# Kernel optimization log

Hardware: AMD Instinct MI355X
Metric: run time of the kernel (lower is better)

The kernel has to match this reference:

```python
import math
import jax, jax.numpy as jnp
import numpy as np

SCALES = (128.0, 256.0, 512.0)
ASPECT_RATIOS = (0.5, 1.0, 2.0)
NMS_THR = 0.7
PRENMS_K = 6000   # rpn_test_prenms_topk (module built with training=False)
POST_K = 300      # rpn_test_topk
MIN_SIZE = 16.0
DW_CLIP = math.log(1000.0 / 16.0)


def conv2d(x, w, b, pad):
    y = jax.lax.conv_general_dilated(
        x, w, window_strides=(1, 1), padding=[(pad, pad), (pad, pad)],
        dimension_numbers=("NCHW", "OIHW", "NCHW"))
    return y + b[None, :, None, None]


def generate_anchors(im_h, im_w, grid_h, grid_w, dtype):
    stride_h = float(im_h // grid_h)
    stride_w = float(im_w // grid_w)
    ar = jnp.asarray(ASPECT_RATIOS, dtype)
    sc = jnp.asarray(SCALES, dtype)
    h_ratios = jnp.sqrt(ar)
    w_ratios = 1.0 / h_ratios
    hs = (h_ratios[:, None] * sc[None, :]).reshape(-1)   # [A]
    ws = (w_ratios[:, None] * sc[None, :]).reshape(-1)
    base = jnp.round(jnp.stack([-ws, -hs, ws, hs], axis=1) / 2.0)  # [A,4]
    xs = jnp.arange(grid_w, dtype=dtype) * stride_w
    ys = jnp.arange(grid_h, dtype=dtype) * stride_h
    sy, sx = jnp.meshgrid(ys, xs, indexing="ij")
    sx = sx.reshape(-1); sy = sy.reshape(-1)
    shift = jnp.stack([sx, sy, sx, sy], axis=1)           # [HW,4]
    return (shift[:, None, :] + base[None, :, :]).reshape(-1, 4)  # [HW*A,4]


def decode_boxes(pred, anchors):
    # pred, anchors: [N,4] -> decoded [N,4]
    w = anchors[:, 2] - anchors[:, 0]
    h = anchors[:, 3] - anchors[:, 1]
    cx = anchors[:, 0] + 0.5 * w
    cy = anchors[:, 1] + 0.5 * h
    dx, dy = pred[:, 0], pred[:, 1]
    dw = jnp.minimum(pred[:, 2], DW_CLIP)
    dh = jnp.minimum(pred[:, 3], DW_CLIP)
    px = dx * w + cx
    py = dy * h + cy
    pw = jnp.exp(dw) * w
    ph = jnp.exp(dh) * h
    return jnp.stack([px - 0.5 * pw, py - 0.5 * ph, px + 0.5 * pw, py + 0.5 * ph], axis=1)


def nms_keep(boxes, valid, thr):
    # boxes assumed sorted by descending score; sequential greedy NMS.
    N = boxes.shape[0]
    area = (boxes[:, 2] - boxes[:, 0]) * (boxes[:, 3] - boxes[:, 1])
    idx = jnp.arange(N)

    def body(i, keep):
        b = jax.lax.dynamic_slice(boxes, (i, 0), (1, 4))[0]
        x1 = jnp.maximum(b[0], boxes[:, 0])
        y1 = jnp.maximum(b[1], boxes[:, 1])
        x2 = jnp.minimum(b[2], boxes[:, 2])
        y2 = jnp.minimum(b[3], boxes[:, 3])
        inter = jnp.clip(x2 - x1, 0.0) * jnp.clip(y2 - y1, 0.0)
        iou = inter / (area[i] + area - inter)
        suppress = (iou > thr) & (idx > i) & keep[i]
        return keep & ~suppress

    return jax.lax.fori_loop(0, N, body, valid)


def rpn_forward(image, feat, rpn_conv_w, rpn_conv_b, cls_w, cls_b, bbox_w, bbox_b):
    rpn_feat = jax.nn.relu(conv2d(feat, rpn_conv_w, rpn_conv_b, pad=1))
    cls_scores = conv2d(rpn_feat, cls_w, cls_b, pad=0)       # [B,A,H,W]
    box_pred = conv2d(rpn_feat, bbox_w, bbox_b, pad=0)       # [B,4A,H,W]
    B, A, H, W = cls_scores.shape
    im_h, im_w = image.shape[-2], image.shape[-1]
    anchors = generate_anchors(im_h, im_w, H, W, feat.dtype)  # [HWA,4]

    cls_flat = jnp.transpose(cls_scores, (0, 2, 3, 1)).reshape(-1)              # [B*H*W*A]
    pred = jnp.transpose(box_pred.reshape(B, A, 4, H, W), (0, 3, 4, 1, 2)).reshape(-1, 4)
    proposals = decode_boxes(pred, anchors)                   # [N,4]

    scores = jax.nn.sigmoid(cls_flat)
    top_scores, top_idx = jax.lax.top_k(scores, PRENMS_K)
    props = proposals[top_idx]                                # [K,4]
    # clamp to image boundary
    props = jnp.stack([
        jnp.clip(props[:, 0], 0.0, float(im_w)),
        jnp.clip(props[:, 1], 0.0, float(im_h)),
        jnp.clip(props[:, 2], 0.0, float(im_w)),
        jnp.clip(props[:, 3], 0.0, float(im_h))], axis=1)
    w = props[:, 2] - props[:, 0]
    h = props[:, 3] - props[:, 1]
    valid = (w >= MIN_SIZE) & (h >= MIN_SIZE)
    keep = nms_keep(props, valid, NMS_THR)                    # already score-sorted
    masked = jnp.where(keep, top_scores, -jnp.inf)
    final_scores, sel = jax.lax.top_k(masked, POST_K)
    final_boxes = props[sel]
    ok = jnp.isfinite(final_scores)
    final_boxes = jnp.where(ok[:, None], final_boxes, 0.0)
    final_scores = jnp.where(ok, final_scores, 0.0)
    return jnp.concatenate([final_boxes, final_scores[:, None]], axis=1)  # [POST_K,5]


def setup_inputs() -> dict:
    key = jax.random.key(0)
    ks = jax.random.split(key, 6)
    C, H, W, A = 256, 128, 128, 9
    IMH = IMW = 1024
    std = 0.01
    return {
        "image": jax.random.normal(ks[0], (1, 3, IMH, IMW), jnp.float32),
        "feat": jax.random.normal(ks[1], (1, C, H, W), jnp.float32),
        "rpn_conv_w": jax.random.normal(ks[2], (C, C, 3, 3), jnp.float32) * std,
        "rpn_conv_b": jnp.zeros((C,), jnp.float32),
        "cls_w": jax.random.normal(ks[3], (A, C, 1, 1), jnp.float32) * std,
        "cls_b": jnp.zeros((A,), jnp.float32),
        "bbox_w": jax.random.normal(ks[4], (4 * A, C, 1, 1), jnp.float32) * std,
        "bbox_b": jnp.zeros((4 * A,), jnp.float32),
    }


def reference(image, feat, rpn_conv_w, rpn_conv_b, cls_w, cls_b, bbox_w, bbox_b):
    return rpn_forward(image, feat, rpn_conv_w, rpn_conv_b, cls_w, cls_b, bbox_w, bbox_b)
```

## Files before the change

### kernel.cpp

```cpp
#include <hip/hip_runtime.h>

#define HW 128
#define NPIX 16384
#define CIN 256
#define NSC 147456
#define PRENMS 6000
#define POSTK 300
#define DW_CLIP_F 4.135166556742356f
#define MW 96
typedef unsigned long long ull;

__global__ void prep_kernel(const float* __restrict__ w, float* __restrict__ wt,
                            const float* __restrict__ cls_w, const float* __restrict__ bbox_w,
                            float* __restrict__ wh45,
                            unsigned* __restrict__ zp, int nz) {
    int i = blockIdx.x * 256 + threadIdx.x;
    if (i < nz) zp[i] = 0u;
    if (i < 11520) {
        int ci = i / 45, s = i - ci * 45;
        wh45[i] = (s < 9) ? cls_w[s * CIN + ci] : bbox_w[(s - 9) * CIN + ci];
    }
    if (i < 2304 * 256) {
        int k = i >> 8, co = i & 255;
        wt[i] = w[co * 2304 + k];
    }
}

__global__ __launch_bounds__(256) void conv3x3_kernel(
    const float* __restrict__ feat, const float* __restrict__ wt,
    float* __restrict__ part)
{
    const int tx = threadIdx.x, ty = threadIdx.y;
    const int x0 = blockIdx.x * 16, y0 = blockIdx.y * 16;
    const int h = blockIdx.z >> 4;
    const int co0 = (blockIdx.z & 15) << 4;
    const int px = x0 + tx, py = y0 + ty;

    float acc[16];
#pragma unroll
    for (int i = 0; i < 16; ++i) acc[i] = 0.f;

    const float* fh = feat + h * 128 * NPIX;
    const float* wh = wt + h * 128 * 9 * 256 + co0;

    const bool interior = (x0 > 0) && (y0 > 0) && (x0 < 112) && (y0 < 112);

    if (interior) {
        const float* fb = fh + (py - 1) * 128 + (px - 1);
#pragma unroll 2
        for (int ci = 0; ci < 128; ++ci) {
            const float* f = fb + ci * NPIX;
            float v[9];
#pragma unroll
            for (int t = 0; t < 9; ++t) {
                const int ky = t / 3, kx = t - ky * 3;
                v[t] = f[ky * 128 + kx];
            }
            const float* wp = wh + ci * 9 * 256;
#pragma unroll
            for (int t = 0; t < 9; ++t) {
#pragma unroll
                for (int co = 0; co < 16; ++co)
                    acc[co] = fmaf(v[t], wp[t * 256 + co], acc[co]);
            }
        }
    } else {
        int off[9];
        float okf[9];
#pragma unroll
        for (int t = 0; t < 9; ++t) {
            const int ky = t / 3 - 1, kx = t - (t / 3) * 3 - 1;
            const int gy = py + ky, gx = px + kx;
            const bool ok = ((unsigned)gy < 128u) && ((unsigned)gx < 128u);
            off[t] = ok ? (gy * 128 + gx) : 0;
            okf[t] = ok ? 1.f : 0.f;
        }
#pragma unroll 2
        for (int ci = 0; ci < 128; ++ci) {
            const float* f = fh + ci * NPIX;
            float v[9];
#pragma unroll
            for (int t = 0; t < 9; ++t) v[t] = f[off[t]] * okf[t];
            const float* wp = wh + ci * 9 * 256;
#pragma unroll
            for (int t = 0; t < 9; ++t) {
#pragma unroll
                for (int co = 0; co < 16; ++co)
                    acc[co] = fmaf(v[t], wp[t * 256 + co], acc[co]);
            }
        }
    }
    float* po = part + h * (CIN * NPIX) + co0 * NPIX + py * 128 + px;
#pragma unroll
    for (int co = 0; co < 16; ++co)
        po[co * NPIX] = acc[co];
}

__global__ __launch_bounds__(256) void heads_kernel(
    const float* __restrict__ part, const float* __restrict__ conv_b,
    const float* __restrict__ wh45,
    const float* __restrict__ cls_b, const float* __restrict__ bbox_b,
    float* __restrict__ scores, float* __restrict__ bb)
{
    __shared__ float partial[3][64][46];
    const int t = threadIdx.x;
    const int lane = t & 63, q = t >> 6;
    const int p = blockIdx.x * 64 + lane;
    const float* p0 = part + p;
    const float* p1 = part + CIN * NPIX + p;
    const int cb = q * 64;

    float acc[45];
#pragma unroll
    for (int i = 0; i < 45; ++i) acc[i] = 0.f;

    float va[4], vb[4];
#pragma unroll
    for (int k = 0; k < 4; ++k) {
        va[k] = p0[(cb + k) * NPIX];
        vb[k] = p1[(cb + k) * NPIX];
    }
#pragma unroll 4
    for (int i = 0; i < 64; ++i) {
        const int ci = cb + i;
        float v = fmaxf(va[i & 3] + vb[i & 3] + conv_b[ci], 0.f);
        if (i + 4 < 64) {
            va[i & 3] = p0[(ci + 4) * NPIX];
            vb[i & 3] = p1[(ci + 4) * NPIX];
        }
        const float* wr = wh45 + ci * 45;
#pragma unroll
        for (int s = 0; s < 45; ++s)
            acc[s] = fmaf(v, wr[s], acc[s]);
    }
    if (q) {
#pragma unroll
        for (int s = 0; s < 45; ++s) partial[q - 1][lane][s] = acc[s];
    }
    __syncthreads();
    if (q == 0) {
#pragma unroll
        for (int s = 0; s < 45; ++s) {
            float r = acc[s] + partial[0][lane][s];
            r += partial[1][lane][s];
            r += partial[2][lane][s];
            acc[s] = r;
        }
#pragma unroll
        for (int a = 0; a < 9; ++a) {
            float s = acc[a] + cls_b[a];
            scores[p * 9 + a] = 1.0f / (1.0f + expf(-s));
        }
#pragma unroll
        for (int c = 0; c < 36; ++c) {
            bb[c * NPIX + p] = acc[9 + c] + bbox_b[c];
        }
    }
}

__global__ __launch_bounds__(1024) void hist1_kernel(const float* __restrict__ scores,
                                                     unsigned* __restrict__ hist1,
                                                     unsigned* __restrict__ meta) {
    __shared__ unsigned h[16384];
    __shared__ unsigned lastflag;
    const int tid = threadIdx.x;
    for (int i = tid; i < 16384; i += 1024) h[i] = 0u;
    __syncthreads();
    for (int i = blockIdx.x * 1024 + tid; i < NSC; i += 64 * 1024) {
        atomicAdd(&h[__float_as_uint(scores[i]) >> 16], 1u);
    }
    __syncthreads();
    for (int i = tid; i < 16384; i += 1024) {
        unsigned c = h[i];
        if (c) atomicAdd(&hist1[i], c);
    }
    __threadfence();
    if (tid == 0) lastflag = (atomicAdd(&meta[4], 1u) == 63u) ? 1u : 0u;
    __syncthreads();
    if (!lastflag) return;
    const volatile unsigned* vh = (const volatile unsigned*)hist1;
    unsigned local[16];
    unsigned s = 0;
#pragma unroll
    for (int i = 0; i < 16; ++i) { local[i] = vh[tid * 16 + i]; s += local[i]; }
    __syncthreads();
    h[tid] = s;
    __syncthreads();
    for (int off = 1; off < 1024; off <<= 1) {
        unsigned v = h[tid] + ((tid + off < 1024) ? h[tid + off] : 0u);
        __syncthreads();
        h[tid] = v;
        __syncthreads();
    }
    unsigned run = h[tid] - s;
#pragma unroll
    for (int i = 15; i >= 0; --i) {
        unsigned nb = run + local[i];
        if (nb >= (unsigned)PRENMS && run < (unsigned)PRENMS) {
            meta[1] = (unsigned)(tid * 16 + i);
            meta[2] = run;
        }
        run = nb;
    }
}

__global__ __launch_bounds__(1024) void hist2_kernel(const float* __restrict__ scores,
                                                     unsigned* __restrict__ meta,
                                                     unsigned* __restrict__ hist2) {
    __shared__ unsigned ss[1024];
    __shared__ unsigned lastflag;
    const int tid = threadIdx.x;
    const unsigned b1 = meta[1];
    for (int i = blockIdx.x * 1024 + tid; i < NSC; i += 64 * 1024) {
        unsigned bits = __float_as_uint(scores[i]);
        if ((bits >> 16) == b1) atomicAdd(&hist2[bits & 0xFFFFu], 1u);
    }
    __threadfence();
    if (tid == 0) lastflag = (atomicAdd(&meta[5], 1u) == 63u) ? 1u : 0u;
    __syncthreads();
    if (!lastflag) return;
    const volatile unsigned* vh = (const volatile unsigned*)hist2;
    const unsigned need = (unsigned)PRENMS - meta[2];
    unsigned local[64];
    unsigned s = 0;
    for (int i = 0; i < 64; ++i) { local[i] = vh[tid * 64 + i]; s += local[i]; }
    ss[tid] = s;
    __syncthreads();
    for (int off = 1; off < 1024; off <<= 1) {
        unsigned v = ss[tid] + ((tid + off < 1024) ? ss[tid + off] : 0u);
        __syncthreads();
        ss[tid] = v;
        __syncthreads();
    }
    unsigned run = ss[tid] - s;
    for (int i = 63; i >= 0; --i) {
        unsigned nb = run + local[i];
        if (nb >= need && run < need) {
            meta[3] = (b1 << 16) | (unsigned)(tid * 64 + i);
        }
        run = nb;
    }
}

__global__ void compact_kernel(const float* __restrict__ scores, unsigned* __restrict__ meta,
                               ull* __restrict__ cand) {
    int i = blockIdx.x * 256 + threadIdx.x;
    unsigned bits = (i < NSC) ? __float_as_uint(scores[i]) : 0u;
    bool pred = (i < NSC) && (bits >= meta[3]);
    ull bal = __ballot(pred);
    int lane = threadIdx.x & 63;
    unsigned cnt = (unsigned)__popcll(bal);
    unsigned base = 0;
    if (lane == 0 && cnt) base = atomicAdd(&meta[0], cnt);
    base = __shfl(base, 0);
    if (pred) {
        unsigned off = (unsigned)__popcll(bal & ((1ull << lane) - 1ull));
        unsigned pos = base + off;
        if (pos < 8192u)
            cand[pos] = ((ull)bits << 32) | (unsigned)(~i);
    }
}

__global__ __launch_bounds__(1024) void sortA_kernel(const ull* __restrict__ cand,
                                                     const unsigned* __restrict__ meta,
                                                     ull* __restrict__ sorted) {
    __shared__ ull keys[2048];
    const int tid = threadIdx.x;
    const int base = blockIdx.x * 2048;
    const int n = min((int)meta[0], 8192);
    for (int i = tid; i < 2048; i += 1024) {
        int g = base + i;
        keys[i] = (g < n) ? cand[g] : (ull)(8191 - g);
    }
    __syncthreads();
    for (int k = 2; k <= 2048; k <<= 1) {
        for (int j = k >> 1; j >= 1; j >>= 1) {
            int s = tid;
            int i = ((s & ~(j - 1)) << 1) | (s & (j - 1));
            int p = i | j;
            ull a = keys[i], c = keys[p];
            bool desc = ((i & k) == 0);
            bool sw = desc ? (a < c) : (a > c);
            if (sw) { keys[i] = c; keys[p] = a; }
            __syncthreads();
        }
    }
    for (int i = tid; i < 2048; i += 1024) sorted[base + i] = keys[i];
}

__global__ __launch_bounds__(256) void merge_decode_kernel(
    const ull* __restrict__ sorted, const float* __restrict__ bb,
    float* __restrict__ selbox, float* __restrict__ selsc,
    ull* __restrict__ validbits)
{
    const int g = blockIdx.x * 256 + threadIdx.x;
    ull key = sorted[g];
    const int c = g >> 11;
    int rank = g & 2047;
#pragma unroll
    for (int cc = 0; cc < 4; ++cc) {
        if (cc == c) continue;
        const ull* arr = sorted + cc * 2048;
        int lo = 0, hi = 2048;
        while (lo < hi) { int mid = (lo + hi) >> 1; if (arr[mid] > key) lo = mid + 1; else hi = mid; }
        rank += lo;
    }
    if (rank >= PRENMS) return;
    unsigned sbits = (unsigned)(key >> 32);
    unsigned idx = ~(unsigned)(key & 0xFFFFFFFFull);
    float score = __uint_as_float(sbits);
    int p = (int)(idx / 9u);
    int a = (int)(idx - (unsigned)p * 9u);
    int y = p >> 7, x = p & 127;
    float d0 = bb[(a * 4 + 0) * NPIX + p];
    float d1 = bb[(a * 4 + 1) * NPIX + p];
    float d2 = bb[(a * 4 + 2) * NPIX + p];
    float d3 = bb[(a * 4 + 3) * NPIX + p];
    int ar_i = a / 3, sc_i = a - ar_i * 3;
    float arv = (ar_i == 0) ? 0.5f : ((ar_i == 1) ? 1.0f : 2.0f);
    float scv = (sc_i == 0) ? 128.f : ((sc_i == 1) ? 256.f : 512.f);
    float hr = sqrtf(arv);
    float wr = 1.0f / hr;
    float hs = hr * scv;
    float wsv = wr * scv;
    float bx1 = rintf(-wsv * 0.5f), by1 = rintf(-hs * 0.5f);
    float bx2 = rintf(wsv * 0.5f),  by2 = rintf(hs * 0.5f);
    float ax1 = x * 8.f + bx1, ay1 = y * 8.f + by1;
    float ax2 = x * 8.f + bx2, ay2 = y * 8.f + by2;
    float wa = ax2 - ax1, ha = ay2 - ay1;
    float cx = ax1 + 0.5f * wa, cy = ay1 + 0.5f * ha;
    float dw = fminf(d2, DW_CLIP_F), dh = fminf(d3, DW_CLIP_F);
    float px = d0 * wa + cx, py = d1 * ha + cy;
    float pw = expf(dw) * wa, ph = expf(dh) * ha;
    float x1 = px - 0.5f * pw, y1 = py - 0.5f * ph;
    float x2 = px + 0.5f * pw, y2 = py + 0.5f * ph;
    x1 = fminf(fmaxf(x1, 0.f), 1024.f);
    y1 = fminf(fmaxf(y1, 0.f), 1024.f);
    x2 = fminf(fmaxf(x2, 0.f), 1024.f);
    y2 = fminf(fmaxf(y2, 0.f), 1024.f);
    float bw = x2 - x1, bh = y2 - y1;
    selbox[rank * 4 + 0] = x1; selbox[rank * 4 + 1] = y1;
    selbox[rank * 4 + 2] = x2; selbox[rank * 4 + 3] = y2;
    selsc[rank] = score;
    if ((bw >= 16.f) && (bh >= 16.f))
        atomicOr(&validbits[rank >> 6], 1ull << (rank & 63));
}

__global__ __launch_bounds__(256) void maskbuild_kernel(
    const float* __restrict__ selbox, ull* __restrict__ mask)
{
    __shared__ float jb0[64], jb1[64], jb2[64], jb3[64];
    const int jw = blockIdx.y;
    const int tid = threadIdx.x;
    const int i = blockIdx.x * 256 + tid;
    if (jw * 64 + 63 < blockIdx.x * 256) {
        if (i < PRENMS) mask[(size_t)i * MW + jw] = 0ull;
        return;
    }
    if (tid < 64) {
        int j = jw * 64 + tid;
        float x1 = 0.f, y1 = 0.f, x2 = 0.f, y2 = 0.f;
        if (j < PRENMS) {
            x1 = selbox[j * 4 + 0]; y1 = selbox[j * 4 + 1];
            x2 = selbox[j * 4 + 2]; y2 = selbox[j * 4 + 3];
        }
        jb0[tid] = x1; jb1[tid] = y1; jb2[tid] = x2; jb3[tid] = y2;
    }
    __syncthreads();
    if (i >= PRENMS) return;
    const float ix1 = selbox[i * 4 + 0], iy1 = selbox[i * 4 + 1];
    const float ix2 = selbox[i * 4 + 2], iy2 = selbox[i * 4 + 3];
    const float iarea = (ix2 - ix1) * (iy2 - iy1);
    ull word = 0ull;
    for (int b = 0; b < 64; ++b) {
        int j = jw * 64 + b;
        float xx1 = fmaxf(ix1, jb0[b]);
        float yy1 = fmaxf(iy1, jb1[b]);
        float xx2 = fminf(ix2, jb2[b]);
        float yy2 = fminf(iy2, jb3[b]);
        float iw = fmaxf(xx2 - xx1, 0.f);
        float ih = fmaxf(yy2 - yy1, 0.f);
        float inter = iw * ih;
        float jarea = (jb2[b] - jb0[b]) * (jb3[b] - jb1[b]);
        float iou = inter / (iarea + jarea - inter);
        if (j > i && iou > 0.7f) word |= (1ull << b);
    }
    mask[(size_t)i * MW + jw] = word;
}

__global__ __launch_bounds__(64) void nms_scan_kernel(
    const ull* __restrict__ validbits,
    const ull* __restrict__ mask,
    const float* __restrict__ selbox, const float* __restrict__ selsc,
    float* __restrict__ out)
{
    __shared__ int kept[POSTK];
    const int l = threadIdx.x;
    ull supp0 = ~validbits[l];
    ull supp1 = (l < 30) ? ~validbits[64 + l] : ~0ull;
    int nk = 0;
    ull ownrow_next = mask[(size_t)l * MW + 0];
    for (int wi = 0; wi < 94 && nk < POSTK; ++wi) {
        ull ownrow = ownrow_next;
        if (wi < 93) ownrow_next = mask[(size_t)((wi + 1) * 64 + l) * MW + (wi + 1)];
        ull wsup = (wi < 64) ? __shfl(supp0, wi) : __shfl(supp1, wi - 64);
        ull active = ~wsup;
        if (!active) continue;
        ull keptbits = 0ull;
        while (active && nk < POSTK) {
            int b = __builtin_ctzll(active);
            keptbits |= (1ull << b);
            if (l == 0) kept[nk] = wi * 64 + b;
            nk++;
            ull rowb = __shfl(ownrow, b);
            ull gt = (b == 63) ? 0ull : (~0ull << (b + 1));
            active &= gt & ~rowb;
        }
        while (keptbits) {
            int b0 = __builtin_ctzll(keptbits); keptbits &= keptbits - 1;
            int b1 = -1, b2 = -1, b3 = -1;
            if (keptbits) { b1 = __builtin_ctzll(keptbits); keptbits &= keptbits - 1; }
            if (keptbits) { b2 = __builtin_ctzll(keptbits); keptbits &= keptbits - 1; }
            if (keptbits) { b3 = __builtin_ctzll(keptbits); keptbits &= keptbits - 1; }
            const ull* r0 = mask + (size_t)(wi * 64 + b0) * MW;
            ull t0a = r0[l], t0b = (l < 30) ? r0[64 + l] : 0ull;
            ull t1a = 0, t1b = 0, t2a = 0, t2b = 0, t3a = 0, t3b = 0;
            if (b1 >= 0) { const ull* r1 = mask + (size_t)(wi * 64 + b1) * MW; t1a = r1[l]; t1b = (l < 30) ? r1[64 + l] : 0ull; }
            if (b2 >= 0) { const ull* r2 = mask + (size_t)(wi * 64 + b2) * MW; t2a = r2[l]; t2b = (l < 30) ? r2[64 + l] : 0ull; }
            if (b3 >= 0) { const ull* r3 = mask + (size_t)(wi * 64 + b3) * MW; t3a = r3[l]; t3b = (l < 30) ? r3[64 + l] : 0ull; }
            supp0 |= t0a | t1a | t2a | t3a;
            supp1 |= t0b | t1b | t2b | t3b;
        }
    }
    __syncthreads();
    for (int r = l; r < POSTK; r += 64) {
        if (r < nk) {
            int i = kept[r];
            out[r * 5 + 0] = selbox[i * 4 + 0];
            out[r * 5 + 1] = selbox[i * 4 + 1];
            out[r * 5 + 2] = selbox[i * 4 + 2];
            out[r * 5 + 3] = selbox[i * 4 + 3];
            out[r * 5 + 4] = selsc[i];
        } else {
            out[r * 5 + 0] = 0.f; out[r * 5 + 1] = 0.f;
            out[r * 5 + 2] = 0.f; out[r * 5 + 3] = 0.f;
            out[r * 5 + 4] = 0.f;
        }
    }
}

extern "C" void kernel_launch(void* const* d_in, const int* in_sizes, int n_in,
                              void* d_out, int out_size, void* d_ws, size_t ws_size,
                              hipStream_t stream) {
    const float* feat    = (const float*)d_in[1];
    const float* conv_w  = (const float*)d_in[2];
    const float* conv_b  = (const float*)d_in[3];
    const float* cls_w   = (const float*)d_in[4];
    const float* cls_b   = (const float*)d_in[5];
    const float* bbox_w  = (const float*)d_in[6];
    const float* bbox_b  = (const float*)d_in[7];
    float* out = (float*)d_out;

    char* ws = (char*)d_ws;
    float*    part      = (float*)(ws + 0);
    float*    wt        = (float*)(ws + 33554432);
    float*    wh45      = (float*)(ws + 35913728);
    float*    bb        = (float*)(ws + 35959808);
    float*    scores    = (float*)(ws + 38319104);
    unsigned* hist1     = (unsigned*)(ws + 38908928);
    unsigned* hist2     = (unsigned*)(ws + 38974464);
    unsigned* meta      = (unsigned*)(ws + 39236608);
    ull*      validbits = (ull*)(ws + 39236864);
    ull*      cand      = (ull*)(ws + 39237632);
    ull*      sorted    = (ull*)(ws + 39303168);
    float*    selbox    = (float*)(ws + 39368704);
    float*    selsc     = (float*)(ws + 39464960);
    ull*      mask      = (ull*)(ws + 39489024);

    const int nz = 16384 + 65536 + 64 + 192;
    prep_kernel<<<2304, 256, 0, stream>>>(conv_w, wt, cls_w, bbox_w, wh45, hist1, nz);
    conv3x3_kernel<<<dim3(8, 8, 32), dim3(16, 16), 0, stream>>>(feat, wt, part);
    heads_kernel<<<256, 256, 0, stream>>>(part, conv_b, wh45, cls_b, bbox_b, scores, bb);
    hist1_kernel<<<64, 1024, 0, stream>>>(scores, hist1, meta);
    hist2_kernel<<<64, 1024, 0, stream>>>(scores, meta, hist2);
    compact_kernel<<<(NSC + 255) / 256, 256, 0, stream>>>(scores, meta, cand);
    sortA_kernel<<<4, 1024, 0, stream>>>(cand, meta, sorted);
    merge_decode_kernel<<<32, 256, 0, stream>>>(sorted, bb, selbox, selsc, validbits);
    maskbuild_kernel<<<dim3(24, 94), 256, 0, stream>>>(selbox, mask);
    nms_scan_kernel<<<1, 64, 0, stream>>>(validbits, mask, selbox, selsc, out);
}
```

Baseline: 623.2 us.

## Stage conv input halo tiles in shared memory across 8-channel chunks

The 3x3 conv kernel now loads an 18x18 halo tile for 8 input channels at a time into LDS and reads the nine taps from shared memory. Before, each thread issued nine global loads per channel and had a separate boundary path. This removes the interior/border split and the redundant global reads of overlapping neighbours, at the cost of two barriers per 8-channel chunk. Extra __syncthreads calls are added before the last-block detection in the histogram kernels, so all of a block's atomics complete before the block counts itself done.

After: 592.6 us. 4.9% less time.

```diff
diff --git a/kernel.cpp b/kernel.cpp
--- a/kernel.cpp
+++ b/kernel.cpp
@@ -26,71 +26,68 @@
     }
 }
 
-__global__ __launch_bounds__(256) void conv3x3_kernel(
+__global__ __launch_bounds__(256) void conv3x3_half_kernel(
     const float* __restrict__ feat, const float* __restrict__ wt,
     float* __restrict__ part)
 {
-    const int tx = threadIdx.x, ty = threadIdx.y;
-    const int x0 = blockIdx.x * 16, y0 = blockIdx.y * 16;
-    const int h = blockIdx.z >> 4;
+    __shared__ float in_s[8 * 324];
+    const int tx = threadIdx.x;
+    const int ty = threadIdx.y;
+    const int x0 = blockIdx.x * 16;
+    const int y0 = blockIdx.y * 16;
+    const int h  = blockIdx.z >> 4;
     const int co0 = (blockIdx.z & 15) << 4;
-    const int px = x0 + tx, py = y0 + ty;
+    const int tid = ty * 16 + tx;
+
+    const int yy1 = tid / 18, xx1 = tid - yy1 * 18;
+    const int t2 = tid + 256;
+    const int yy2 = t2 / 18, xx2 = t2 - yy2 * 18;
+    const int gy1 = y0 + yy1 - 1, gx1 = x0 + xx1 - 1;
+    const int gy2 = y0 + yy2 - 1, gx2 = x0 + xx2 - 1;
+    const bool p1 = ((unsigned)gy1 < 128u) && ((unsigned)gx1 < 128u);
+    const bool p2 = (tid < 68) && ((unsigned)gy2 < 128u) && ((unsigned)gx2 < 128u);
+    const int a1 = p1 ? (gy1 * 128 + gx1) : 0;
+    const int a2 = p2 ? (gy2 * 128 + gx2) : 0;
 
     float acc[16];
 #pragma unroll
     for (int i = 0; i < 16; ++i) acc[i] = 0.f;
 
     const float* fh = feat + h * 128 * NPIX;
-    const float* wh = wt + h * 128 * 9 * 256 + co0;
-
-    const bool interior = (x0 > 0) && (y0 > 0) && (x0 < 112) && (y0 < 112);
-
-    if (interior) {
-        const float* fb = fh + (py - 1) * 128 + (px - 1);
-#pragma unroll 2
-        for (int ci = 0; ci < 128; ++ci) {
-            const float* f = fb + ci * NPIX;
-            float v[9];
+    const float* wh = wt + h * 128 * 9 * 256;
+
+    for (int s = 0; s < 16; ++s) {
+        __syncthreads();
+        const float* fbase = fh + s * 8 * NPIX;
+#pragma unroll
+        for (int ci = 0; ci < 8; ++ci) {
+            float t = fbase[ci * NPIX + a1];
+            in_s[ci * 324 + tid] = p1 ? t : 0.f;
+        }
+        if (tid < 68) {
+#pragma unroll
+            for (int ci = 0; ci < 8; ++ci) {
+                float t = fbase[ci * NPIX + a2];
+                in_s[ci * 324 + 256 + tid] = p2 ? t : 0.f;
+            }
+        }
+        __syncthreads();
+        const float* ws0 = wh + s * 8 * 9 * 256 + co0;
+#pragma unroll 4
+        for (int ci = 0; ci < 8; ++ci) {
+            const float* wrow = ws0 + ci * 9 * 256;
 #pragma unroll
             for (int t = 0; t < 9; ++t) {
                 const int ky = t / 3, kx = t - ky * 3;
-                v[t] = f[ky * 128 + kx];
+                float v = in_s[ci * 324 + (ty + ky) * 18 + (tx + kx)];
+                const float* wp = wrow + t * 256;
+#pragma unroll
+                for (int co = 0; co < 16; ++co)
+                    acc[co] = fmaf(v, wp[co], acc[co]);
             }
-            const float* wp = wh + ci * 9 * 256;
-#pragma unroll
-            for (int t = 0; t < 9; ++t) {
-#pragma unroll
-                for (int co = 0; co < 16; ++co)
-                    acc[co] = fmaf(v[t], wp[t * 256 + co], acc[co]);
-            }
-        }
-    } else {
-        int off[9];
-        float okf[9];
-#pragma unroll
-        for (int t = 0; t < 9; ++t) {
-            const int ky = t / 3 - 1, kx = t - (t / 3) * 3 - 1;
-            const int gy = py + ky, gx = px + kx;
-            const bool ok = ((unsigned)gy < 128u) && ((unsigned)gx < 128u);
-            off[t] = ok ? (gy * 128 + gx) : 0;
-            okf[t] = ok ? 1.f : 0.f;
-        }
-#pragma unroll 2
-        for (int ci = 0; ci < 128; ++ci) {
-            const float* f = fh + ci * NPIX;
-            float v[9];
-#pragma unroll
-            for (int t = 0; t < 9; ++t) v[t] = f[off[t]] * okf[t];
-            const float* wp = wh + ci * 9 * 256;
-#pragma unroll
-            for (int t = 0; t < 9; ++t) {
-#pragma unroll
-                for (int co = 0; co < 16; ++co)
-                    acc[co] = fmaf(v[t], wp[t * 256 + co], acc[co]);
-            }
-        }
-    }
-    float* po = part + h * (CIN * NPIX) + co0 * NPIX + py * 128 + px;
+        }
+    }
+    float* po = part + h * (CIN * NPIX) + co0 * NPIX + (y0 + ty) * 128 + (x0 + tx);
 #pragma unroll
     for (int co = 0; co < 16; ++co)
         po[co * NPIX] = acc[co];
@@ -174,6 +171,7 @@
         unsigned c = h[i];
         if (c) atomicAdd(&hist1[i], c);
     }
+    __syncthreads();
     __threadfence();
     if (tid == 0) lastflag = (atomicAdd(&meta[4], 1u) == 63u) ? 1u : 0u;
     __syncthreads();
@@ -215,6 +213,7 @@
         unsigned bits = __float_as_uint(scores[i]);
         if ((bits >> 16) == b1) atomicAdd(&hist2[bits & 0xFFFFu], 1u);
     }
+    __syncthreads();
     __threadfence();
     if (tid == 0) lastflag = (atomicAdd(&meta[5], 1u) == 63u) ? 1u : 0u;
     __syncthreads();
@@ -479,7 +478,7 @@
 
     const int nz = 16384 + 65536 + 64 + 192;
     prep_kernel<<<2304, 256, 0, stream>>>(conv_w, wt, cls_w, bbox_w, wh45, hist1, nz);
-    conv3x3_kernel<<<dim3(8, 8, 32), dim3(16, 16), 0, stream>>>(feat, wt, part);
+    conv3x3_half_kernel<<<dim3(8, 8, 32), dim3(16, 16), 0, stream>>>(feat, wt, part);
     heads_kernel<<<256, 256, 0, stream>>>(part, conv_b, wh45, cls_b, bbox_b, scores, bb);
     hist1_kernel<<<64, 1024, 0, stream>>>(scores, hist1, meta);
     hist2_kernel<<<64, 1024, 0, stream>>>(scores, meta, hist2);
```
